# Performance work log

Measured on AMD Instinct MI355X. Metric: run time of the kernel, lower is better.

## Reference

```python
import jax, jax.numpy as jnp
import numpy as np

# Model dims (from HF weight layout in docstring)
B, S, HID = 2, 2048, 2048
HV, HK, DK, DV = 32, 16, 128, 128      # v-heads, k-heads, key head dim, value head dim
KEY_DIM = HK * DK                      # 2048
VAL_DIM = HV * DV                      # 4096
CONV_DIM = 2 * KEY_DIM + VAL_DIM       # 8192
KS = 4                                 # causal conv kernel size
EPS = 1e-6                             # l2norm + rmsnorm eps


def setup_inputs() -> dict:
    key = jax.random.key(0)
    ks = jax.random.split(key, 8)
    s = lambda k, shape, scale: jax.random.normal(k, shape, dtype=jnp.float32) * scale
    return {
        "hidden_states": s(ks[0], (B, S, HID), 1.0),
        "W_qkv": s(ks[1], (CONV_DIM, HID), 0.02),
        "W_z": s(ks[2], (VAL_DIM, HID), 0.02),
        "W_a": s(ks[3], (HV, HID), 0.02),
        "W_b": s(ks[4], (HV, HID), 0.02),
        "conv_w": s(ks[5], (CONV_DIM, KS), 0.2),
        "A_log": jnp.zeros((HV,), jnp.float32),
        "dt_bias": jnp.ones((HV,), jnp.float32),
        "norm_w": jnp.ones((DV,), jnp.float32),
        "W_out": s(ks[6], (HID, VAL_DIM), 0.02),
    }


def _l2norm(x):
    return x / jnp.maximum(jnp.linalg.norm(x, axis=-1, keepdims=True), EPS)


def reference(hidden_states, W_qkv, W_z, W_a, W_b, conv_w, A_log, dt_bias, norm_w, W_out):
    Bn, Sn, _ = hidden_states.shape
    # input projections
    qkv = hidden_states @ W_qkv.T            # (B,S,CONV_DIM) -- already [q|k|v] order
    z = hidden_states @ W_z.T                # (B,S,VAL_DIM)
    a = hidden_states @ W_a.T                # (B,S,HV)
    b = hidden_states @ W_b.T                # (B,S,HV)
    # causal depthwise conv1d over time (padding=KS-1 on the left), then SiLU
    xp = jnp.pad(qkv, ((0, 0), (KS - 1, 0), (0, 0)))
    conv = sum(xp[:, k:k + Sn, :] * conv_w[:, k] for k in range(KS))
    mixed = jax.nn.silu(conv)                # (B,S,CONV_DIM)
    # split into heads; expand K heads to V heads (repeat-interleave)
    q = mixed[..., :KEY_DIM].reshape(Bn, Sn, HK, DK)
    k = mixed[..., KEY_DIM:2 * KEY_DIM].reshape(Bn, Sn, HK, DK)
    v = mixed[..., 2 * KEY_DIM:].reshape(Bn, Sn, HV, DV)
    rep = HV // HK
    q = jnp.repeat(q, rep, axis=2)           # (B,S,HV,DK)
    k = jnp.repeat(k, rep, axis=2)
    q = _l2norm(q) * (DK ** -0.5)
    k = _l2norm(k)
    # gates: log-decay g and write gate beta
    g = -jnp.exp(A_log) * jax.nn.softplus(a + dt_bias)   # (B,S,HV), <= 0
    beta = jax.nn.sigmoid(b)                              # (B,S,HV)
    # delta-rule recurrence over sequence (scan over time)
    qs = q.transpose(1, 0, 2, 3)   # (S,B,H,DK)
    ks_ = k.transpose(1, 0, 2, 3)
    vs = v.transpose(1, 0, 2, 3)   # (S,B,H,DV)
    gs = g.transpose(1, 0, 2)
    bs = beta.transpose(1, 0, 2)

    def step(state, inp):
        qt, kt, vt, gt, bt = inp
        state = state * jnp.exp(gt)[..., None, None]                 # decay
        kv = jnp.einsum('bhk,bhkv->bhv', kt, state)                  # read memory
        delta = (vt - kv) * bt[..., None]                            # gated delta
        state = state + jnp.einsum('bhk,bhv->bhkv', kt, delta)       # rank-1 write
        out = jnp.einsum('bhk,bhkv->bhv', qt, state)                 # query read
        return state, out

    state0 = jnp.zeros((Bn, HV, DK, DV), hidden_states.dtype)
    _, outs = jax.lax.scan(step, state0, (qs, ks_, vs, gs, bs))
    o = outs.transpose(1, 0, 2, 3)                                   # (B,S,HV,DV)
    # gated per-head RMSNorm, then output projection
    var = jnp.mean(jnp.square(o), axis=-1, keepdims=True)
    o = o * jax.lax.rsqrt(var + EPS) * norm_w
    o = o * jax.nn.silu(z.reshape(Bn, Sn, HV, DV))
    return o.reshape(Bn, Sn, VAL_DIM) @ W_out.T                      # (B,S,HID)
```

## Files before the change

### kernel.cpp

```cpp
#include <hip/hip_runtime.h>
#include <math.h>

typedef unsigned short u16;
typedef __attribute__((ext_vector_type(8))) short short8;
typedef __attribute__((ext_vector_type(4))) float f32x4;

#define EPS 1e-6f
#define AS1(p) ((const __attribute__((address_space(1))) void*)(p))
#define AS3(p) ((__attribute__((address_space(3))) void*)(p))

__device__ __forceinline__ unsigned f2bf(float f) {
  union { float f; unsigned u; } v; v.f = f;
  return (v.u + 0x7fffu + ((v.u >> 16) & 1u)) >> 16;
}
__device__ __forceinline__ float bf2f(u16 u) {
  union { unsigned u; float f; } v; v.u = ((unsigned)u) << 16; return v.f;
}

__global__ void k_cvt(const float* __restrict__ in, u16* __restrict__ out, int n) {
  int i = (blockIdx.x * blockDim.x + threadIdx.x) * 4;
  if (i >= n) return;
  float4 v = *(const float4*)(in + i);
  uint2 p;
  p.x = f2bf(v.x) | (f2bf(v.y) << 16);
  p.y = f2bf(v.z) | (f2bf(v.w) << 16);
  *(uint2*)(out + i) = p;
}

template <bool OB>
__global__ __launch_bounds__(256) void k_gemm_bt(const u16* __restrict__ A,
                                                 const u16* __restrict__ Bm,
                                                 void* __restrict__ Cv,
                                                 int M, int N, int K) {
  __shared__ short sA[4096];
  __shared__ short sB[4096];
  const int tid = threadIdx.x;
  const int w = tid >> 6, lane = tid & 63;
  const int nbt = N >> 7;
  const int nwg = (M >> 7) * nbt;
  int bid = blockIdx.x;
  {
    int q = nwg >> 3;
    bid = (bid & 7) * q + (bid >> 3);
  }
  const int mt = bid / nbt, nt = bid - mt * nbt;
  const int m0 = mt << 7, n0 = nt << 7;
  const int wr = (w >> 1) << 6, wc = (w & 1) << 6;

  f32x4 acc[4][4] = {};

  int rdA[4], rdB[4];
#pragma unroll
  for (int i = 0; i < 4; ++i) {
    int row = wr + i * 16 + (lane & 15);
    rdA[i] = row * 64 + (((lane >> 4) ^ ((row >> 1) & 3)) << 4);
    int col = wc + i * 16 + (lane & 15);
    rdB[i] = col * 64 + (((lane >> 4) ^ ((col >> 1) & 3)) << 4);
  }
  int srow[2], scol[2];
#pragma unroll
  for (int j = 0; j < 2; ++j) {
    int y = (w * 2 + j) * 1024 + lane * 16;
    int rr = y >> 6;
    int cs = ((y >> 4) & 3) ^ ((rr >> 1) & 3);
    srow[j] = rr;
    scol[j] = cs * 8;
  }
  const int nk = K >> 5;
  for (int kt = 0; kt < nk; ++kt) {
    const int k0 = kt << 5;
#pragma unroll
    for (int j = 0; j < 2; ++j) {
      const int ca = (w * 2 + j) * 1024;
      const u16* ga = A + (size_t)(m0 + srow[j]) * K + (k0 + scol[j]);
      __builtin_amdgcn_global_load_lds(AS1(ga), AS3((char*)sA + ca), 16, 0, 0);
      const u16* gb = Bm + (size_t)(n0 + srow[j]) * K + (k0 + scol[j]);
      __builtin_amdgcn_global_load_lds(AS1(gb), AS3((char*)sB + ca), 16, 0, 0);
    }
    __syncthreads();
    short8 af[4], bfr[4];
#pragma unroll
    for (int i = 0; i < 4; ++i) af[i] = *(const short8*)((const char*)sA + rdA[i]);
#pragma unroll
    for (int i = 0; i < 4; ++i) bfr[i] = *(const short8*)((const char*)sB + rdB[i]);
#pragma unroll
    for (int i = 0; i < 4; ++i)
#pragma unroll
      for (int j = 0; j < 4; ++j)
        acc[i][j] = __builtin_amdgcn_mfma_f32_16x16x32_bf16(af[i], bfr[j], acc[i][j], 0, 0, 0);
    __syncthreads();
  }
#pragma unroll
  for (int i = 0; i < 4; ++i)
#pragma unroll
    for (int j = 0; j < 4; ++j)
#pragma unroll
      for (int qe = 0; qe < 4; ++qe) {
        int mrow = m0 + wr + i * 16 + ((lane >> 4) << 2) + qe;
        int ncol = n0 + wc + j * 16 + (lane & 15);
        if (OB) ((u16*)Cv)[(size_t)mrow * N + ncol] = (u16)f2bf(acc[i][j][qe]);
        else    ((float*)Cv)[(size_t)mrow * N + ncol] = acc[i][j][qe];
      }
}

__global__ void k_gates(const float* __restrict__ hidden, const float* __restrict__ Wa,
                        const float* __restrict__ Wb, const float* __restrict__ Alog,
                        const float* __restrict__ dtb, float* __restrict__ g,
                        float* __restrict__ beta) {
  int t = blockIdx.x;
  int tid = threadIdx.x;
  int h = tid & 31;
  const float4* h4 = (const float4*)(hidden + (size_t)t * 2048);
  const float4* w4 = (const float4*)((tid < 32 ? Wa : Wb) + (size_t)h * 2048);
  float acc = 0.f;
  for (int i = 0; i < 512; ++i) {
    float4 x = h4[i], y = w4[i];
    acc += x.x * y.x + x.y * y.y + x.z * y.z + x.w * y.w;
  }
  if (tid < 32) {
    float x = acc + dtb[h];
    float sp = x > 20.f ? x : log1pf(expf(x));
    g[t * 32 + h] = -expf(Alog[h]) * sp;
  } else {
    beta[t * 32 + h] = 1.f / (1.f + expf(-acc));
  }
}

__global__ __launch_bounds__(256) void k_conv(const u16* __restrict__ qkv,
                                              const float* __restrict__ convw,
                                              u16* __restrict__ qnb, u16* __restrict__ knb,
                                              u16* __restrict__ vvb) {
  __shared__ float mix[4096];
  __shared__ float red[32][8];
  __shared__ float fac[32];
  const int t = blockIdx.x;
  const int s = t & 2047;
  const int tid = threadIdx.x;
  const u16* base = qkv + (size_t)t * 8192;
  for (int it = 0; it < 2; ++it) {
    int c0 = (it * 256 + tid) * 8;
    short8 x0 = *(const short8*)(base + c0);
    short8 x1 = (short8)0, x2 = (short8)0, x3 = (short8)0;
    if (s >= 1) x1 = *(const short8*)(base + c0 - 8192);
    if (s >= 2) x2 = *(const short8*)(base + c0 - 16384);
    if (s >= 3) x3 = *(const short8*)(base + c0 - 24576);
#pragma unroll
    for (int e = 0; e < 8; ++e) {
      int c = c0 + e;
      float4 wv = *(const float4*)(convw + c * 4);
      float a = bf2f((u16)x0[e]) * wv.w + bf2f((u16)x1[e]) * wv.z
              + bf2f((u16)x2[e]) * wv.y + bf2f((u16)x3[e]) * wv.x;
      mix[c] = a / (1.f + expf(-a));
    }
  }
  for (int it = 0; it < 2; ++it) {
    int c0 = 4096 + (it * 256 + tid) * 8;
    short8 x0 = *(const short8*)(base + c0);
    short8 x1 = (short8)0, x2 = (short8)0, x3 = (short8)0;
    if (s >= 1) x1 = *(const short8*)(base + c0 - 8192);
    if (s >= 2) x2 = *(const short8*)(base + c0 - 16384);
    if (s >= 3) x3 = *(const short8*)(base + c0 - 24576);
    unsigned pk[4];
#pragma unroll
    for (int e2 = 0; e2 < 4; ++e2) {
      float vs[2];
#pragma unroll
      for (int u = 0; u < 2; ++u) {
        int e = e2 * 2 + u;
        float4 wv = *(const float4*)(convw + (c0 + e) * 4);
        float a = bf2f((u16)x0[e]) * wv.w + bf2f((u16)x1[e]) * wv.z
                + bf2f((u16)x2[e]) * wv.y + bf2f((u16)x3[e]) * wv.x;
        vs[u] = a / (1.f + expf(-a));
      }
      pk[e2] = f2bf(vs[0]) | (f2bf(vs[1]) << 16);
    }
    *(uint4*)(vvb + (size_t)t * 4096 + (c0 - 4096)) = *(uint4*)pk;
  }
  __syncthreads();
  {
    int hh = tid >> 3, p = tid & 7;
    float ss2 = 0.f;
#pragma unroll
    for (int e = 0; e < 16; ++e) { float x = mix[hh * 128 + p * 16 + e]; ss2 += x * x; }
    red[hh][p] = ss2;
  }
  __syncthreads();
  if (tid < 32) {
    float ss2 = 0.f;
#pragma unroll
    for (int p = 0; p < 8; ++p) ss2 += red[tid][p];
    float inv = 1.f / fmaxf(sqrtf(ss2), EPS);
    if (tid < 16) inv *= 0.08838834764831845f;
    fac[tid] = inv;
  }
  __syncthreads();
  for (int it = 0; it < 2; ++it) {
    int c0 = (it * 256 + tid) * 8;
    float f = fac[c0 >> 7];
    unsigned pk[4];
#pragma unroll
    for (int e2 = 0; e2 < 4; ++e2) {
      float v0 = mix[c0 + e2 * 2] * f;
      float v1 = mix[c0 + e2 * 2 + 1] * f;
      pk[e2] = f2bf(v0) | (f2bf(v1) << 16);
    }
    if (it == 0) *(uint4*)(qnb + (size_t)t * 2048 + c0)          = *(uint4*)pk;
    else         *(uint4*)(knb + (size_t)t * 2048 + (c0 - 2048)) = *(uint4*)pk;
  }
}

#define CH 64
__global__ __launch_bounds__(256) void k_recur(const u16* __restrict__ qn,
                                               const u16* __restrict__ kn,
                                               const u16* __restrict__ vv,
                                               const float* __restrict__ g,
                                               const float* __restrict__ beta,
                                               u16* __restrict__ o) {
  __shared__ u16 sk[CH * 128];
  __shared__ u16 sq[CH * 128];
  __shared__ float seg[CH];
  __shared__ float sbe[CH];
  __shared__ float part1[2][4][32];
  __shared__ float part2[2][4][32];
  const int bid = blockIdx.x;
  const int b = bid >> 7, h = (bid >> 2) & 31, qtr = bid & 3;
  const int hk = h >> 1;
  const int tid = threadIdx.x, w = tid >> 6, lane = tid & 63;
  const int col = qtr * 32 + (lane & 31);
  const int r0 = w * 32 + (lane >> 5) * 16;
  float st[16] = {};
  const u16* kbase = kn + ((size_t)b * 2048 * 16 + hk) * 128;
  const u16* qbase = qn + ((size_t)b * 2048 * 16 + hk) * 128;
  const float* gbase = g + (size_t)b * 2048 * 32 + h;
  const float* bbase = beta + (size_t)b * 2048 * 32 + h;
  const u16* vbase = vv + ((size_t)b * 2048 * 32 + h) * 128 + col;
  u16* obase = o + ((size_t)b * 2048 * 32 + h) * 128 + col;

  for (int ch = 0; ch < 2048 / CH; ++ch) {
    const int s0 = ch * CH;
    __syncthreads();
#pragma unroll
    for (int j = 0; j < 4; ++j) {
      const int u = j * 4096 + w * 1024;
      const int y = u + lane * 16;
      const int stp = y >> 8;
      const int d = (y & 255) >> 1;
      const u16* gk = kbase + (size_t)(s0 + stp) * 2048 + d;
      __builtin_amdgcn_global_load_lds(AS1(gk), AS3((char*)sk + u), 16, 0, 0);
      const u16* gq = qbase + (size_t)(s0 + stp) * 2048 + d;
      __builtin_amdgcn_global_load_lds(AS1(gq), AS3((char*)sq + u), 16, 0, 0);
    }
    if (tid < CH) seg[tid] = expf(gbase[(size_t)(s0 + tid) * 32]);
    else if (tid < 2 * CH) sbe[tid - CH] = bbase[(size_t)(s0 + tid - CH) * 32];
    __syncthreads();
#pragma unroll 1
    for (int i = 0; i < CH; ++i) {
      const int s = s0 + i;
      const float eg = seg[i], bet = sbe[i];
      const float vval = bf2f(vbase[(size_t)s * 4096]);
      short8 kr0 = *(const short8*)(sk + i * 128 + r0);
      short8 kr1 = *(const short8*)(sk + i * 128 + r0 + 8);
      short8 qr0 = *(const short8*)(sq + i * 128 + r0);
      short8 qr1 = *(const short8*)(sq + i * 128 + r0 + 8);
      float kk[16], qq[16];
#pragma unroll
      for (int e = 0; e < 8; ++e) {
        kk[e] = bf2f((u16)kr0[e]); kk[8 + e] = bf2f((u16)kr1[e]);
        qq[e] = bf2f((u16)qr0[e]); qq[8 + e] = bf2f((u16)qr1[e]);
      }
      float kvp = 0.f;
#pragma unroll
      for (int tt = 0; tt < 16; ++tt) { st[tt] *= eg; kvp += kk[tt] * st[tt]; }
      kvp += __shfl_xor(kvp, 32);
      const int pb = i & 1;
      if (lane < 32) part1[pb][w][lane] = kvp;
      __syncthreads();
      const int c31 = lane & 31;
      float kv = part1[pb][0][c31] + part1[pb][1][c31] + part1[pb][2][c31] + part1[pb][3][c31];
      float delta = (vval - kv) * bet;
      float op = 0.f;
#pragma unroll
      for (int tt = 0; tt < 16; ++tt) { st[tt] += kk[tt] * delta; op += qq[tt] * st[tt]; }
      op += __shfl_xor(op, 32);
      if (lane < 32) part2[pb][w][lane] = op;
      __syncthreads();
      if (tid < 32) {
        float ov = part2[pb][0][tid] + part2[pb][1][tid] + part2[pb][2][tid] + part2[pb][3][tid];
        obase[(size_t)s * 4096] = (u16)f2bf(ov);
      }
    }
  }
}

__global__ __launch_bounds__(256) void k_epi(const u16* __restrict__ o,
                                             const u16* __restrict__ z,
                                             const float* __restrict__ nw,
                                             u16* __restrict__ og) {
  int gw = (blockIdx.x * 256 + threadIdx.x) >> 6;
  int lane = threadIdx.x & 63;
  size_t base = (size_t)gw * 128;
  int d = lane * 2;
  unsigned xp = *(const unsigned*)(o + base + d);
  float x0 = bf2f((u16)(xp & 0xffff));
  float x1 = bf2f((u16)(xp >> 16));
  float ss = x0 * x0 + x1 * x1;
#pragma unroll
  for (int off = 1; off < 64; off <<= 1) ss += __shfl_xor(ss, off);
  float rms = rsqrtf(ss * (1.f / 128.f) + EPS);
  unsigned zp = *(const unsigned*)(z + base + d);
  float z0 = bf2f((u16)(zp & 0xffff));
  float z1 = bf2f((u16)(zp >> 16));
  float s0 = z0 / (1.f + expf(-z0));
  float s1 = z1 / (1.f + expf(-z1));
  float v0 = x0 * rms * nw[d] * s0;
  float v1 = x1 * rms * nw[d + 1] * s1;
  *(unsigned*)(og + base + d) = f2bf(v0) | (f2bf(v1) << 16);
}

extern "C" void kernel_launch(void* const* d_in, const int* in_sizes, int n_in,
                              void* d_out, int out_size, void* d_ws, size_t ws_size,
                              hipStream_t stream) {
  const float* hidden = (const float*)d_in[0];
  const float* Wqkv   = (const float*)d_in[1];
  const float* Wz     = (const float*)d_in[2];
  const float* Wa     = (const float*)d_in[3];
  const float* Wb     = (const float*)d_in[4];
  const float* convw  = (const float*)d_in[5];
  const float* Alog   = (const float*)d_in[6];
  const float* dtb    = (const float*)d_in[7];
  const float* nw     = (const float*)d_in[8];
  const float* Wout   = (const float*)d_in[9];

  char* ws = (char*)d_ws;
  size_t off = 0;
  auto take = [&](size_t b) { char* p = ws + off; off += (b + 255) & ~(size_t)255; return p; };
  u16* hb    = (u16*)take(8388608ull * 2);
  u16* wreg  = (u16*)take(16777216ull * 2);
  u16* qkvb  = (u16*)take(33554432ull * 2);
  u16* vvb   = (u16*)take(16777216ull * 2);
  float* gg  = (float*)take(131072ull * 4);
  float* bb  = (float*)take(131072ull * 4);
  u16* qnb = wreg;
  u16* knb = wreg + 8388608;
  u16* wzb = qkvb + 16777216;
  u16* oob = qkvb;
  u16* zb  = vvb;
  u16* wob = wreg;
  u16* og  = qkvb + 16777216;

  k_cvt<<<8192, 256, 0, stream>>>(hidden, hb, 8388608);
  k_cvt<<<16384, 256, 0, stream>>>(Wqkv, wreg, 16777216);
  k_gemm_bt<true><<<2048, 256, 0, stream>>>(hb, wreg, qkvb, 4096, 8192, 2048);
  k_gates<<<4096, 64, 0, stream>>>(hidden, Wa, Wb, Alog, dtb, gg, bb);
  k_conv<<<4096, 256, 0, stream>>>(qkvb, convw, qnb, knb, vvb);
  k_cvt<<<8192, 256, 0, stream>>>(Wz, wzb, 8388608);
  k_recur<<<256, 256, 0, stream>>>(qnb, knb, vvb, gg, bb, oob);
  k_gemm_bt<true><<<1024, 256, 0, stream>>>(hb, wzb, zb, 4096, 4096, 2048);
  k_cvt<<<8192, 256, 0, stream>>>(Wout, wob, 8388608);
  k_epi<<<32768, 256, 0, stream>>>(oob, zb, nw, og);
  k_gemm_bt<false><<<512, 256, 0, stream>>>(og, wob, d_out, 4096, 2048, 4096);
}
```

Measured before the change: 1.996 ms.

## Restructure recurrence into single-wavefront blocks with double-buffered LDS staging

The recurrence kernel now uses one 64-lane wavefront per block, each handling 8 value columns of a head, and launches 1024 blocks instead of 256. The per-step cross-wave reductions through shared memory and __syncthreads are replaced by in-wave shuffle reductions. The k/q/v/gate chunks are staged asynchronously into double-buffered LDS so the loads for the next chunk overlap compute, and the block index is swizzled. Each block still reloads the full k and q rows, so global and LDS traffic for k/q grows with the number of column groups.

```diff
diff --git a/kernel.cpp b/kernel.cpp
--- a/kernel.cpp
+++ b/kernel.cpp
@@ -209,86 +209,100 @@
   }
 }
 
-#define CH 64
-__global__ __launch_bounds__(256) void k_recur(const u16* __restrict__ qn,
-                                               const u16* __restrict__ kn,
-                                               const u16* __restrict__ vv,
-                                               const float* __restrict__ g,
-                                               const float* __restrict__ beta,
-                                               u16* __restrict__ o) {
-  __shared__ u16 sk[CH * 128];
-  __shared__ u16 sq[CH * 128];
-  __shared__ float seg[CH];
-  __shared__ float sbe[CH];
-  __shared__ float part1[2][4][32];
-  __shared__ float part2[2][4][32];
-  const int bid = blockIdx.x;
-  const int b = bid >> 7, h = (bid >> 2) & 31, qtr = bid & 3;
-  const int hk = h >> 1;
-  const int tid = threadIdx.x, w = tid >> 6, lane = tid & 63;
-  const int col = qtr * 32 + (lane & 31);
-  const int r0 = w * 32 + (lane >> 5) * 16;
-  float st[16] = {};
+#define RCH 32
+__global__ __launch_bounds__(64) void k_recur(const u16* __restrict__ qn,
+                                              const u16* __restrict__ kn,
+                                              const u16* __restrict__ vv,
+                                              const float* __restrict__ g,
+                                              const float* __restrict__ beta,
+                                              u16* __restrict__ o) {
+  __shared__ u16 sk[2][RCH * 128];
+  __shared__ u16 sq[2][RCH * 128];
+  __shared__ u16 sv[2][RCH * 8];
+  __shared__ float sG[2][RCH];
+  __shared__ float sBt[2][RCH];
+  int bid = blockIdx.x;
+  const int swz = (bid & 7) * 128 + (bid >> 3);
+  const int b = swz >> 9, h = (swz >> 4) & 31, cg = swz & 15;
+  const int hk = h >> 1, c0 = cg * 8;
+  const int lane = threadIdx.x & 63;
+  const int oct = lane >> 3, ci = lane & 7;
   const u16* kbase = kn + ((size_t)b * 2048 * 16 + hk) * 128;
   const u16* qbase = qn + ((size_t)b * 2048 * 16 + hk) * 128;
   const float* gbase = g + (size_t)b * 2048 * 32 + h;
   const float* bbase = beta + (size_t)b * 2048 * 32 + h;
-  const u16* vbase = vv + ((size_t)b * 2048 * 32 + h) * 128 + col;
-  u16* obase = o + ((size_t)b * 2048 * 32 + h) * 128 + col;
-
-  for (int ch = 0; ch < 2048 / CH; ++ch) {
-    const int s0 = ch * CH;
+  const u16* vbase = vv + ((size_t)b * 2048 * 32 + h) * 128 + c0;
+  u16* obase = o + ((size_t)b * 2048 * 32 + h) * 128 + c0 + ci;
+
+  float st[16] = {};
+
+  auto stage = [&](int s0, int ib) {
+#pragma unroll
+    for (int j = 0; j < 8; ++j) {
+      const int y = j * 1024 + lane * 16;
+      const int stp = y >> 8, dc = (y & 255) >> 1;
+      __builtin_amdgcn_global_load_lds(AS1(kbase + (size_t)(s0 + stp) * 2048 + dc),
+                                       AS3((char*)sk[ib] + j * 1024), 16, 0, 0);
+      __builtin_amdgcn_global_load_lds(AS1(qbase + (size_t)(s0 + stp) * 2048 + dc),
+                                       AS3((char*)sq[ib] + j * 1024), 16, 0, 0);
+    }
+    if (lane < RCH) {
+      __builtin_amdgcn_global_load_lds(AS1(vbase + (size_t)(s0 + lane) * 4096),
+                                       AS3((char*)sv[ib]), 16, 0, 0);
+      sG[ib][lane] = expf(gbase[(size_t)(s0 + lane) * 32]);
+    } else {
+      sBt[ib][lane - RCH] = bbase[(size_t)(s0 + lane - RCH) * 32];
+    }
+  };
+
+  stage(0, 0);
+  __syncthreads();
+  for (int ch = 0; ch < 2048 / RCH; ++ch) {
+    const int ib = ch & 1;
+    if (ch + 1 < 2048 / RCH) stage((ch + 1) * RCH, ib ^ 1);
+#pragma unroll 4
+    for (int i = 0; i < RCH; ++i) {
+      const int s = ch * RCH + i;
+      const float eg = sG[ib][i], bet = sBt[ib][i];
+      const float vval = bf2f(sv[ib][i * 8 + ci]);
+      const u16* kr = &sk[ib][i * 128 + oct * 16];
+      const u16* qr = &sq[ib][i * 128 + oct * 16];
+      short8 k0 = *(const short8*)kr, k1 = *(const short8*)(kr + 8);
+      short8 q0 = *(const short8*)qr, q1 = *(const short8*)(qr + 8);
+      float kk[16], qq[16];
+#pragma unroll
+      for (int e = 0; e < 8; ++e) {
+        kk[e] = bf2f((u16)k0[e]); kk[8 + e] = bf2f((u16)k1[e]);
+        qq[e] = bf2f((u16)q0[e]); qq[8 + e] = bf2f((u16)q1[e]);
+      }
+      float a0 = 0.f, a1 = 0.f, a2 = 0.f, a3 = 0.f;
+#pragma unroll
+      for (int t4 = 0; t4 < 16; t4 += 4) {
+        st[t4 + 0] *= eg; a0 += kk[t4 + 0] * st[t4 + 0];
+        st[t4 + 1] *= eg; a1 += kk[t4 + 1] * st[t4 + 1];
+        st[t4 + 2] *= eg; a2 += kk[t4 + 2] * st[t4 + 2];
+        st[t4 + 3] *= eg; a3 += kk[t4 + 3] * st[t4 + 3];
+      }
+      float kv = (a0 + a1) + (a2 + a3);
+      kv += __shfl_xor(kv, 8);
+      kv += __shfl_xor(kv, 16);
+      kv += __shfl_xor(kv, 32);
+      const float delta = (vval - kv) * bet;
+      float o0 = 0.f, o1 = 0.f, o2 = 0.f, o3 = 0.f;
+#pragma unroll
+      for (int t4 = 0; t4 < 16; t4 += 4) {
+        st[t4 + 0] += kk[t4 + 0] * delta; o0 += qq[t4 + 0] * st[t4 + 0];
+        st[t4 + 1] += kk[t4 + 1] * delta; o1 += qq[t4 + 1] * st[t4 + 1];
+        st[t4 + 2] += kk[t4 + 2] * delta; o2 += qq[t4 + 2] * st[t4 + 2];
+        st[t4 + 3] += kk[t4 + 3] * delta; o3 += qq[t4 + 3] * st[t4 + 3];
+      }
+      float op = (o0 + o1) + (o2 + o3);
+      op += __shfl_xor(op, 8);
+      op += __shfl_xor(op, 16);
+      op += __shfl_xor(op, 32);
+      if (oct == 0) obase[(size_t)s * 4096] = (u16)f2bf(op);
+    }
     __syncthreads();
-#pragma unroll
-    for (int j = 0; j < 4; ++j) {
-      const int u = j * 4096 + w * 1024;
-      const int y = u + lane * 16;
-      const int stp = y >> 8;
-      const int d = (y & 255) >> 1;
-      const u16* gk = kbase + (size_t)(s0 + stp) * 2048 + d;
-      __builtin_amdgcn_global_load_lds(AS1(gk), AS3((char*)sk + u), 16, 0, 0);
-      const u16* gq = qbase + (size_t)(s0 + stp) * 2048 + d;
-      __builtin_amdgcn_global_load_lds(AS1(gq), AS3((char*)sq + u), 16, 0, 0);
-    }
-    if (tid < CH) seg[tid] = expf(gbase[(size_t)(s0 + tid) * 32]);
-    else if (tid < 2 * CH) sbe[tid - CH] = bbase[(size_t)(s0 + tid - CH) * 32];
-    __syncthreads();
-#pragma unroll 1
-    for (int i = 0; i < CH; ++i) {
-      const int s = s0 + i;
-      const float eg = seg[i], bet = sbe[i];
-      const float vval = bf2f(vbase[(size_t)s * 4096]);
-      short8 kr0 = *(const short8*)(sk + i * 128 + r0);
-      short8 kr1 = *(const short8*)(sk + i * 128 + r0 + 8);
-      short8 qr0 = *(const short8*)(sq + i * 128 + r0);
-      short8 qr1 = *(const short8*)(sq + i * 128 + r0 + 8);
-      float kk[16], qq[16];
-#pragma unroll
-      for (int e = 0; e < 8; ++e) {
-        kk[e] = bf2f((u16)kr0[e]); kk[8 + e] = bf2f((u16)kr1[e]);
-        qq[e] = bf2f((u16)qr0[e]); qq[8 + e] = bf2f((u16)qr1[e]);
-      }
-      float kvp = 0.f;
-#pragma unroll
-      for (int tt = 0; tt < 16; ++tt) { st[tt] *= eg; kvp += kk[tt] * st[tt]; }
-      kvp += __shfl_xor(kvp, 32);
-      const int pb = i & 1;
-      if (lane < 32) part1[pb][w][lane] = kvp;
-      __syncthreads();
-      const int c31 = lane & 31;
-      float kv = part1[pb][0][c31] + part1[pb][1][c31] + part1[pb][2][c31] + part1[pb][3][c31];
-      float delta = (vval - kv) * bet;
-      float op = 0.f;
-#pragma unroll
-      for (int tt = 0; tt < 16; ++tt) { st[tt] += kk[tt] * delta; op += qq[tt] * st[tt]; }
-      op += __shfl_xor(op, 32);
-      if (lane < 32) part2[pb][w][lane] = op;
-      __syncthreads();
-      if (tid < 32) {
-        float ov = part2[pb][0][tid] + part2[pb][1][tid] + part2[pb][2][tid] + part2[pb][3][tid];
-        obase[(size_t)s * 4096] = (u16)f2bf(ov);
-      }
-    }
   }
 }
 
@@ -354,7 +368,7 @@
   k_gates<<<4096, 64, 0, stream>>>(hidden, Wa, Wb, Alog, dtb, gg, bb);
   k_conv<<<4096, 256, 0, stream>>>(qkvb, convw, qnb, knb, vvb);
   k_cvt<<<8192, 256, 0, stream>>>(Wz, wzb, 8388608);
-  k_recur<<<256, 256, 0, stream>>>(qnb, knb, vvb, gg, bb, oob);
+  k_recur<<<1024, 64, 0, stream>>>(qnb, knb, vvb, gg, bb, oob);
   k_gemm_bt<true><<<1024, 256, 0, stream>>>(hb, wzb, zb, 4096, 4096, 2048);
   k_cvt<<<8192, 256, 0, stream>>>(Wout, wob, 8388608);
   k_epi<<<32768, 256, 0, stream>>>(oob, zb, nw, og);
```

New measurement: 1.904 ms. 4.6% less time.
